# Kernel optimization log

Hardware: AMD Instinct MI355X
Metric: run time of the kernel (lower is better)

Reference implementation:

```python
import jax, jax.numpy as jnp
import numpy as np

D_MODEL = 256
N_HEADS = 8
N_LEVELS = 4
N_POINTS = 4
D_FFN = 1024
HW = 128
LQ = HW * HW
LIN = N_LEVELS * LQ
BATCH = 2
HEAD_DIM = D_MODEL // N_HEADS
SPATIAL = [(HW, HW)] * N_LEVELS  # static (H, W) per level
EPS = 1e-5


def _layer_norm(x, g, b):
    m = jnp.mean(x, axis=-1, keepdims=True)
    v = jnp.mean(jnp.square(x - m), axis=-1, keepdims=True)
    return (x - m) * jax.lax.rsqrt(v + EPS) * g + b


def _gather(v, idx):
    # v: (N, heads, HW, hd); idx: (N, heads, Lq, P) -> (N, heads, Lq, P, hd)
    N, Hh, Lq, P = idx.shape
    out = jnp.take_along_axis(v, idx.reshape(N, Hh, Lq * P)[..., None], axis=2)
    return out.reshape(N, Hh, Lq, P, -1)


def _ms_deform_attn_core(value, loc, attn):
    # value: (N, Lin, heads, hd); loc: (N, Lq, heads, L, P, 2) in [0,1]; attn: (N, Lq, heads, L, P)
    N, _, Hh, hd = value.shape
    Lq = loc.shape[1]
    out = jnp.zeros((N, Hh, Lq, hd), value.dtype)
    start = 0
    for l, (H, W) in enumerate(SPATIAL):
        v = value[:, start:start + H * W].transpose(0, 2, 1, 3)  # (N, heads, H*W, hd)
        start += H * W
        ll = loc[:, :, :, l].transpose(0, 2, 1, 3, 4)  # (N, heads, Lq, P, 2)
        # F.grid_sample(align_corners=False, padding_mode='zeros') on grid 2*loc-1:
        # pixel coord = loc * size - 0.5
        x = ll[..., 0] * W - 0.5
        y = ll[..., 1] * H - 0.5
        x0 = jnp.floor(x)
        y0 = jnp.floor(y)
        wx = x - x0
        wy = y - y0
        x0i = x0.astype(jnp.int32)
        y0i = y0.astype(jnp.int32)
        acc = jnp.zeros((N, Hh, Lq, N_POINTS, hd), value.dtype)
        for dy, wyc in ((0, 1.0 - wy), (1, wy)):
            for dx, wxc in ((0, 1.0 - wx), (1, wx)):
                xi = x0i + dx
                yi = y0i + dy
                valid = (xi >= 0) & (xi < W) & (yi >= 0) & (yi < H)
                idx = jnp.clip(yi, 0, H - 1) * W + jnp.clip(xi, 0, W - 1)
                g = _gather(v, idx)
                w = (wxc * wyc * valid).astype(value.dtype)
                acc = acc + g * w[..., None]
        aw = attn[:, :, :, l].transpose(0, 2, 1, 3)  # (N, heads, Lq, P)
        out = out + jnp.sum(acc * aw[..., None], axis=3)
    return out.transpose(0, 2, 1, 3).reshape(N, Lq, Hh * hd)


def _forward(cur_src, src_all, pos, reference_points, spatial_shape,
             W_off, b_off, W_attn, b_attn, W_val, b_val, W_out, b_out,
             gamma1, beta1, W1, b1, W2, b2, gamma2, beta2):
    N, Lq, d = cur_src.shape
    q = cur_src + pos[:, -1]                      # with_pos_embed(cur_src, pos[-1])
    inp = src_all + pos.reshape(N, -1, d)         # with_pos_embed(src_all, cat(pos, 1))
    value = (inp @ W_val + b_val).reshape(N, -1, N_HEADS, HEAD_DIM)
    off = (q @ W_off + b_off).reshape(N, Lq, N_HEADS, N_LEVELS, N_POINTS, 2)
    attn = (q @ W_attn + b_attn).reshape(N, Lq, N_HEADS, N_LEVELS * N_POINTS)
    attn = jax.nn.softmax(attn, axis=-1).reshape(N, Lq, N_HEADS, N_LEVELS, N_POINTS)
    # offset_normalizer = stack([W, H], -1)
    normalizer = jnp.stack([spatial_shape[..., 1], spatial_shape[..., 0]], -1).astype(cur_src.dtype)
    loc = reference_points[:, :, None, :, None, :] + off / normalizer[None, None, None, :, None, :]
    src2 = _ms_deform_attn_core(value, loc, attn) @ W_out + b_out
    src = _layer_norm(cur_src + src2, gamma1, beta1)   # dropout is identity in eval
    ffn = jax.nn.relu(src @ W1 + b1) @ W2 + b2
    return _layer_norm(src + ffn, gamma2, beta2)


def setup_inputs():
    key = jax.random.key(0)
    ks = jax.random.split(key, 16)
    s = 0.02
    f32 = jnp.float32
    return {
        "cur_src": jax.random.normal(ks[0], (BATCH, LQ, D_MODEL), f32),
        "src_all": jax.random.normal(ks[1], (BATCH, LIN, D_MODEL), f32),
        "pos": jax.random.normal(ks[2], (BATCH, N_LEVELS, LQ, D_MODEL), f32),
        "reference_points": jax.random.uniform(ks[3], (BATCH, LQ, N_LEVELS, 2), f32),
        "spatial_shape": jnp.array(SPATIAL, dtype=jnp.int32),
        "level_start_index": (jnp.arange(N_LEVELS) * LQ).astype(jnp.int32),
        "W_off": jax.random.normal(ks[4], (D_MODEL, N_HEADS * N_LEVELS * N_POINTS * 2), f32) * s,
        "b_off": jax.random.normal(ks[5], (N_HEADS * N_LEVELS * N_POINTS * 2,), f32) * 0.5,
        "W_attn": jax.random.normal(ks[6], (D_MODEL, N_HEADS * N_LEVELS * N_POINTS), f32) * s,
        "b_attn": jnp.zeros((N_HEADS * N_LEVELS * N_POINTS,), f32),
        "W_val": jax.random.normal(ks[7], (D_MODEL, D_MODEL), f32) * s,
        "b_val": jnp.zeros((D_MODEL,), f32),
        "W_out": jax.random.normal(ks[8], (D_MODEL, D_MODEL), f32) * s,
        "b_out": jnp.zeros((D_MODEL,), f32),
        "gamma1": jnp.ones((D_MODEL,), f32),
        "beta1": jnp.zeros((D_MODEL,), f32),
        "W1": jax.random.normal(ks[9], (D_MODEL, D_FFN), f32) * s,
        "b1": jnp.zeros((D_FFN,), f32),
        "W2": jax.random.normal(ks[10], (D_FFN, D_MODEL), f32) * s,
        "b2": jnp.zeros((D_MODEL,), f32),
        "gamma2": jnp.ones((D_MODEL,), f32),
        "beta2": jnp.zeros((D_MODEL,), f32),
    }


def reference(cur_src, src_all, pos, reference_points, spatial_shape, level_start_index,
              W_off, b_off, W_attn, b_attn, W_val, b_val, W_out, b_out,
              gamma1, beta1, W1, b1, W2, b2, gamma2, beta2):
    return _forward(cur_src, src_all, pos, reference_points, spatial_shape,
                    W_off, b_off, W_attn, b_attn, W_val, b_val, W_out, b_out,
                    gamma1, beta1, W1, b1, W2, b2, gamma2, beta2)
```

## Files before the change

kernel.cpp:

```cpp
#include <hip/hip_runtime.h>

#define LQN   16384
#define LINN  65536

typedef __attribute__((ext_vector_type(8))) short bf16x8;
typedef __attribute__((ext_vector_type(4))) float f32x4;
typedef __attribute__((ext_vector_type(4))) unsigned short bf16x4;

__device__ __forceinline__ unsigned short f2bf(float f) {
  unsigned u = __float_as_uint(f);
  u += 0x7FFFu + ((u >> 16) & 1u);
  return (unsigned short)(u >> 16);
}

__global__ __launch_bounds__(256) void wtrans6_kernel(
    const float* __restrict__ Wv, const float* __restrict__ Wo,
    const float* __restrict__ Wa, const float* __restrict__ Wu,
    const float* __restrict__ W1, const float* __restrict__ W2,
    unsigned short* __restrict__ wt) {
  int idx = blockIdx.x * 256 + threadIdx.x;
  const float* W; int K, N, base;
  if (idx < 131072) {
    if (idx < 65536) { W = Wv; K = 256; N = 256; base = 0; }
    else             { W = Wo; K = 256; N = 256; base = 65536; }
  } else if (idx < 229376) {
    if (idx < 163840) { W = Wa; K = 256; N = 128; base = 131072; }
    else              { W = Wu; K = 256; N = 256; base = 163840; }
  } else if (idx < 491520) { W = W1; K = 256; N = 1024; base = 229376; }
  else                     { W = W2; K = 1024; N = 256; base = 491520; }
  int local = idx - base;
  int n = local / K, k = local - n * K;
  wt[idx] = f2bf(W[(size_t)k * N + n]);
}

__global__ __launch_bounds__(256) void addcvt_kernel(
    const float* __restrict__ src_all, const float* __restrict__ pos,
    const float* __restrict__ cur, unsigned short* __restrict__ inp_bf,
    unsigned short* __restrict__ qb) {
  size_t i = (size_t)blockIdx.x * 256 + threadIdx.x;
  if (i < 8388608) {
    float4 a = ((const float4*)src_all)[i];
    float4 b = ((const float4*)pos)[i];
    bf16x4 o;
    o.x = f2bf(a.x + b.x); o.y = f2bf(a.y + b.y);
    o.z = f2bf(a.z + b.z); o.w = f2bf(a.w + b.w);
    ((bf16x4*)inp_bf)[i] = o;
  } else {
    size_t j = i - 8388608;
    size_t row = j >> 6;
    int n = (int)(row >> 14), lq = (int)(row & 16383);
    float4 a = ((const float4*)cur)[j];
    float4 b = ((const float4*)pos)[(((size_t)n * 4 + 3) * LQN + lq) * 64 + (j & 63)];
    bf16x4 o;
    o.x = f2bf(a.x + b.x); o.y = f2bf(a.y + b.y);
    o.z = f2bf(a.z + b.z); o.w = f2bf(a.w + b.w);
    ((bf16x4*)qb)[j] = o;
  }
}

template <int DO_RELU, int OUT_BF16, int SPLIT>
__global__ __launch_bounds__(256) void gemm_lds_kernel(
    const unsigned short* __restrict__ A, const unsigned short* __restrict__ Bt,
    const float* __restrict__ bias, const float* __restrict__ bias2,
    void* __restrict__ Cp, float* __restrict__ Cp2,
    int M, int N, int K, int ny) {
  __shared__ unsigned short As[128 * 64];
  __shared__ unsigned short Bs[128 * 64];
  const int bid = blockIdx.x;
  const int by = bid % ny, bx = bid / ny;
  const int m0 = bx * 128, n0 = by * 128;
  const int tid = threadIdx.x;
  const int wave = tid >> 6, lane = tid & 63;
  const int wm = (wave >> 1) * 64, wn = (wave & 1) * 64;
  const int l15 = lane & 15, quad = lane >> 4;
  const int rl = lane >> 3;
  const int cl = (lane & 7) ^ rl;

  f32x4 acc[4][4];
#pragma unroll
  for (int i = 0; i < 4; i++)
#pragma unroll
    for (int j = 0; j < 4; j++)
#pragma unroll
      for (int r = 0; r < 4; r++) acc[i][j][r] = 0.f;

  const unsigned short* Abase = A + (size_t)m0 * K + cl * 8;
  const unsigned short* Bbase = Bt + (size_t)n0 * K + cl * 8;

  for (int k0 = 0; k0 < K; k0 += 64) {
#pragma unroll
    for (int t = 0; t < 4; t++) {
      const int row = wave * 32 + t * 8 + rl;
      __builtin_amdgcn_global_load_lds(
          (const __attribute__((address_space(1))) void*)(Abase + (size_t)row * K + k0),
          (__attribute__((address_space(3))) void*)(As + (wave * 32 + t * 8) * 64),
          16, 0, 0);
      __builtin_amdgcn_global_load_lds(
          (const __attribute__((address_space(1))) void*)(Bbase + (size_t)row * K + k0),
          (__attribute__((address_space(3))) void*)(Bs + (wave * 32 + t * 8) * 64),
          16, 0, 0);
    }
    __syncthreads();
#pragma unroll
    for (int kk = 0; kk < 2; kk++) {
      bf16x8 af[4], bfr[4];
#pragma unroll
      for (int i = 0; i < 4; i++) {
        const int row = wm + i * 16 + l15;
        af[i] = *(const bf16x8*)&As[row * 64 + (((quad + 4 * kk) ^ (row & 7)) * 8)];
      }
#pragma unroll
      for (int j = 0; j < 4; j++) {
        const int row = wn + j * 16 + l15;
        bfr[j] = *(const bf16x8*)&Bs[row * 64 + (((quad + 4 * kk) ^ (row & 7)) * 8)];
      }
#pragma unroll
      for (int i = 0; i < 4; i++)
#pragma unroll
        for (int j = 0; j < 4; j++)
          acc[i][j] = __builtin_amdgcn_mfma_f32_16x16x32_bf16(af[i], bfr[j], acc[i][j], 0, 0, 0);
    }
    __syncthreads();
  }
#pragma unroll
  for (int i = 0; i < 4; i++) {
#pragma unroll
    for (int j = 0; j < 4; j++) {
      const int col = n0 + wn + j * 16 + l15;
      float bv;
      if (SPLIT) bv = (col < 256) ? bias[col] : bias2[col - 256];
      else       bv = bias[col];
#pragma unroll
      for (int r = 0; r < 4; r++) {
        const int row = m0 + wm + i * 16 + quad * 4 + r;
        float v = acc[i][j][r] + bv;
        if (DO_RELU) v = fmaxf(v, 0.f);
        if (SPLIT) {
          if (col < 256) ((float*)Cp)[(size_t)row * 256 + col] = v;
          else           Cp2[(size_t)row * 128 + (col - 256)] = v;
        } else if (OUT_BF16) {
          ((unsigned short*)Cp)[(size_t)row * N + col] = f2bf(v);
        } else {
          ((float*)Cp)[(size_t)row * N + col] = v;
        }
      }
    }
  }
}

__global__ __launch_bounds__(256) void sample_kernel(
    const unsigned short* __restrict__ value, const float* __restrict__ offs,
    const float* __restrict__ attnl, const float* __restrict__ refp,
    unsigned int* __restrict__ attn_out) {
  const int tid = threadIdx.x;
  const int sub = tid >> 4;
  const int c = tid & 15;
  const int g = blockIdx.x * 16 + sub;
  const int n = g >> 17;
  const int nl = g >> 3;
  const int h = g & 7;

  const float* lg = attnl + (size_t)nl * 128 + h * 16;
  float e[16];
  float mx = -1e30f;
#pragma unroll
  for (int i = 0; i < 16; i++) { e[i] = lg[i]; mx = fmaxf(mx, e[i]); }
  float s = 0.f;
#pragma unroll
  for (int i = 0; i < 16; i++) { e[i] = __expf(e[i] - mx); s += e[i]; }
  const float inv = 1.f / s;

  const int pt = c;
  const int pl = pt >> 2;
  const float ox = offs[((size_t)g * 16 + pt) * 2 + 0];
  const float oy = offs[((size_t)g * 16 + pt) * 2 + 1];
  const float rx = refp[((size_t)nl * 4 + pl) * 2 + 0];
  const float ry = refp[((size_t)nl * 4 + pl) * 2 + 1];
  const float x = fmaf(rx, 128.f, ox - 0.5f);
  const float y = fmaf(ry, 128.f, oy - 0.5f);
  const float xf = floorf(x), yf = floorf(y);
  const float fx = x - xf, fy = y - yf;
  const int x0 = (int)xf, y0 = (int)yf;
  const float aw = e[pt] * inv;
  const int xc0 = min(max(x0, 0), 127), xc1 = min(max(x0 + 1, 0), 127);
  const int yc0 = min(max(y0, 0), 127), yc1 = min(max(y0 + 1, 0), 127);
  float wx0 = (x0 >= 0 && x0 <= 127) ? (1.f - fx) : 0.f;
  float wx1 = (x0 >= -1 && x0 <= 126) ? fx : 0.f;
  float wy0 = ((y0 >= 0 && y0 <= 127) ? (1.f - fy) : 0.f) * aw;
  float wy1 = ((y0 >= -1 && y0 <= 126) ? fy : 0.f) * aw;
  const int packed = xc0 | (xc1 << 7) | (yc0 << 14) | (yc1 << 21);

  const unsigned int* base0 =
      (const unsigned int*)value + (((size_t)n * LINN) * 8 + h) * 16 + c;

  float a0 = 0.f, a1 = 0.f;
#pragma unroll
  for (int p = 0; p < 16; p++) {
    const int pk = __shfl(packed, p, 16);
    const float w_x0 = __shfl(wx0, p, 16);
    const float w_x1 = __shfl(wx1, p, 16);
    const float w_y0 = __shfl(wy0, p, 16);
    const float w_y1 = __shfl(wy1, p, 16);
    const unsigned int* bl = base0 + (size_t)(p >> 2) * (LQN * 128);
    const int X0 = pk & 127, X1 = (pk >> 7) & 127;
    const int Y0 = (pk >> 14) & 127, Y1 = (pk >> 21) & 127;
    const unsigned v00 = bl[(Y0 * 128 + X0) * 128];
    const unsigned v01 = bl[(Y0 * 128 + X1) * 128];
    const unsigned v10 = bl[(Y1 * 128 + X0) * 128];
    const unsigned v11 = bl[(Y1 * 128 + X1) * 128];
    const float w00 = w_x0 * w_y0, w01 = w_x1 * w_y0;
    const float w10 = w_x0 * w_y1, w11 = w_x1 * w_y1;
    a0 = fmaf(w00, __uint_as_float(v00 << 16), a0);
    a1 = fmaf(w00, __uint_as_float(v00 & 0xFFFF0000u), a1);
    a0 = fmaf(w01, __uint_as_float(v01 << 16), a0);
    a1 = fmaf(w01, __uint_as_float(v01 & 0xFFFF0000u), a1);
    a0 = fmaf(w10, __uint_as_float(v10 << 16), a0);
    a1 = fmaf(w10, __uint_as_float(v10 & 0xFFFF0000u), a1);
    a0 = fmaf(w11, __uint_as_float(v11 << 16), a0);
    a1 = fmaf(w11, __uint_as_float(v11 & 0xFFFF0000u), a1);
  }
  attn_out[(size_t)g * 16 + c] = (unsigned)f2bf(a0) | ((unsigned)f2bf(a1) << 16);
}

template <int EMIT_BF16>
__global__ __launch_bounds__(256) void ln_kernel(const float* __restrict__ x1,
                                                 const float* __restrict__ x2,
                                                 const float* __restrict__ gamma,
                                                 const float* __restrict__ beta,
                                                 float* __restrict__ out,
                                                 unsigned short* __restrict__ outb) {
  const int row = blockIdx.x * 4 + (threadIdx.x >> 6);
  const int lane = threadIdx.x & 63;
  float4 a = ((const float4*)(x1 + (size_t)row * 256))[lane];
  float4 b = ((const float4*)(x2 + (size_t)row * 256))[lane];
  float v0 = a.x + b.x, v1 = a.y + b.y, v2 = a.z + b.z, v3 = a.w + b.w;
  float s1 = v0 + v1 + v2 + v3;
  float s2 = v0 * v0 + v1 * v1 + v2 * v2 + v3 * v3;
#pragma unroll
  for (int o = 1; o < 64; o <<= 1) { s1 += __shfl_xor(s1, o); s2 += __shfl_xor(s2, o); }
  const float mean = s1 * (1.f / 256.f);
  const float var = s2 * (1.f / 256.f) - mean * mean;
  const float rstd = rsqrtf(var + 1e-5f);
  float4 gm = ((const float4*)gamma)[lane];
  float4 bt = ((const float4*)beta)[lane];
  float4 o4;
  o4.x = (v0 - mean) * rstd * gm.x + bt.x;
  o4.y = (v1 - mean) * rstd * gm.y + bt.y;
  o4.z = (v2 - mean) * rstd * gm.z + bt.z;
  o4.w = (v3 - mean) * rstd * gm.w + bt.w;
  ((float4*)(out + (size_t)row * 256))[lane] = o4;
  if (EMIT_BF16) {
    bf16x4 ob;
    ob.x = f2bf(o4.x); ob.y = f2bf(o4.y); ob.z = f2bf(o4.z); ob.w = f2bf(o4.w);
    ((bf16x4*)(outb + (size_t)row * 256))[lane] = ob;
  }
}

extern "C" void kernel_launch(void* const* d_in, const int* in_sizes, int n_in,
                              void* d_out, int out_size, void* d_ws, size_t ws_size,
                              hipStream_t stream) {
  (void)in_sizes; (void)n_in; (void)out_size; (void)ws_size;
  const float* cur_src = (const float*)d_in[0];
  const float* src_all = (const float*)d_in[1];
  const float* pos     = (const float*)d_in[2];
  const float* refp    = (const float*)d_in[3];
  const float* W_off   = (const float*)d_in[6];
  const float* b_off   = (const float*)d_in[7];
  const float* W_attn  = (const float*)d_in[8];
  const float* b_attn  = (const float*)d_in[9];
  const float* W_val   = (const float*)d_in[10];
  const float* b_val   = (const float*)d_in[11];
  const float* W_out   = (const float*)d_in[12];
  const float* b_out   = (const float*)d_in[13];
  const float* gamma1  = (const float*)d_in[14];
  const float* beta1   = (const float*)d_in[15];
  const float* W1      = (const float*)d_in[16];
  const float* b1      = (const float*)d_in[17];
  const float* W2      = (const float*)d_in[18];
  const float* b2      = (const float*)d_in[19];
  const float* gamma2  = (const float*)d_in[20];
  const float* beta2   = (const float*)d_in[21];
  float* out = (float*)d_out;

  char* ws = (char*)d_ws;
  unsigned short* value = (unsigned short*)(ws + 0);
  unsigned short* qbuf  = (unsigned short*)(ws + 67108864);
  float* offbuf         = (float*)(ws + 83886080);
  float* attnl          = (float*)(ws + 117440512);
  unsigned short* attno = (unsigned short*)(ws + 134217728);
  float* src2           = (float*)(ws + 150994944);
  float* srcb           = (float*)(ws + 184549376);
  unsigned short* wt    = (unsigned short*)(ws + 218103808);
  unsigned short* wt_val  = wt;
  unsigned short* wt_qa   = wt + 65536;
  unsigned short* wt_out  = wt + 163840;
  unsigned short* wt_1    = wt + 229376;
  unsigned short* wt_2    = wt + 491520;
  unsigned short* srcb_bf = (unsigned short*)attnl;
  unsigned short* inp_bf  = (unsigned short*)src2;

  wtrans6_kernel<<<2944, 256, 0, stream>>>(W_val, W_off, W_attn, W_out, W1, W2, wt);

  addcvt_kernel<<<40960, 256, 0, stream>>>(src_all, pos, cur_src, inp_bf, qbuf);

  gemm_lds_kernel<0, 1, 0><<<2048, 256, 0, stream>>>(
      inp_bf, wt_val, b_val, nullptr, value, nullptr, 131072, 256, 256, 2);
  gemm_lds_kernel<0, 0, 1><<<768, 256, 0, stream>>>(
      qbuf, wt_qa, b_off, b_attn, offbuf, attnl, 32768, 384, 256, 3);
  sample_kernel<<<16384, 256, 0, stream>>>(value, offbuf, attnl, refp,
                                           (unsigned int*)attno);
  gemm_lds_kernel<0, 0, 0><<<512, 256, 0, stream>>>(
      attno, wt_out, b_out, nullptr, src2, nullptr, 32768, 256, 256, 2);
  ln_kernel<1><<<8192, 256, 0, stream>>>(cur_src, src2, gamma1, beta1, srcb, srcb_bf);
  gemm_lds_kernel<1, 1, 0><<<2048, 256, 0, stream>>>(
      srcb_bf, wt_1, b1, nullptr, value, nullptr, 32768, 1024, 256, 8);
  gemm_lds_kernel<0, 0, 0><<<512, 256, 0, stream>>>(
      value, wt_2, b2, nullptr, offbuf, nullptr, 32768, 256, 1024, 2);
  ln_kernel<0><<<8192, 256, 0, stream>>>(srcb, offbuf, gamma2, beta2, out, nullptr);
}
```

Before: 643.4 us.

## Restructure deformable sampling to 8 lanes per head with LDS-staged weights and wider loads

The sampling kernel now assigns 8 lanes per (query, head), each handling 4 channels with 8-byte loads. Per-point bilinear weights and packed corner indices are staged in LDS instead of being broadcast through shuffles, and softmax is computed by a cooperative shuffle reduction. The goal is fewer load instructions and less shuffle/ALU overhead on the gather-bound stage. The add-and-convert kernel also reuses the already-loaded pos value for the query buffer, which removes a separate grid region and a second pos read, at the cost of some added LDS use.

```diff
diff --git a/kernel.cpp b/kernel.cpp
--- a/kernel.cpp
+++ b/kernel.cpp
@@ -38,23 +38,20 @@
     const float* __restrict__ cur, unsigned short* __restrict__ inp_bf,
     unsigned short* __restrict__ qb) {
   size_t i = (size_t)blockIdx.x * 256 + threadIdx.x;
-  if (i < 8388608) {
-    float4 a = ((const float4*)src_all)[i];
-    float4 b = ((const float4*)pos)[i];
-    bf16x4 o;
-    o.x = f2bf(a.x + b.x); o.y = f2bf(a.y + b.y);
-    o.z = f2bf(a.z + b.z); o.w = f2bf(a.w + b.w);
-    ((bf16x4*)inp_bf)[i] = o;
-  } else {
-    size_t j = i - 8388608;
-    size_t row = j >> 6;
-    int n = (int)(row >> 14), lq = (int)(row & 16383);
-    float4 a = ((const float4*)cur)[j];
-    float4 b = ((const float4*)pos)[(((size_t)n * 4 + 3) * LQN + lq) * 64 + (j & 63)];
-    bf16x4 o;
-    o.x = f2bf(a.x + b.x); o.y = f2bf(a.y + b.y);
-    o.z = f2bf(a.z + b.z); o.w = f2bf(a.w + b.w);
-    ((bf16x4*)qb)[j] = o;
+  float4 a = ((const float4*)src_all)[i];
+  float4 b = ((const float4*)pos)[i];
+  bf16x4 o;
+  o.x = f2bf(a.x + b.x); o.y = f2bf(a.y + b.y);
+  o.z = f2bf(a.z + b.z); o.w = f2bf(a.w + b.w);
+  ((bf16x4*)inp_bf)[i] = o;
+  size_t m = i & 4194303;
+  if (m >= 3145728) {
+    size_t jq = (i >> 22) * 1048576 + (m - 3145728);
+    float4 cc = ((const float4*)cur)[jq];
+    bf16x4 o2;
+    o2.x = f2bf(cc.x + b.x); o2.y = f2bf(cc.y + b.y);
+    o2.z = f2bf(cc.z + b.z); o2.w = f2bf(cc.w + b.w);
+    ((bf16x4*)qb)[jq] = o2;
   }
 }
 
@@ -152,74 +149,87 @@
     const unsigned short* __restrict__ value, const float* __restrict__ offs,
     const float* __restrict__ attnl, const float* __restrict__ refp,
     unsigned int* __restrict__ attn_out) {
+  __shared__ float wlds[32 * 16 * 8];
   const int tid = threadIdx.x;
-  const int sub = tid >> 4;
-  const int c = tid & 15;
-  const int g = blockIdx.x * 16 + sub;
+  const int sub = tid >> 3;
+  const int cl  = tid & 7;
+  const int g = blockIdx.x * 32 + sub;
   const int n = g >> 17;
   const int nl = g >> 3;
   const int h = g & 7;
 
   const float* lg = attnl + (size_t)nl * 128 + h * 16;
-  float e[16];
-  float mx = -1e30f;
-#pragma unroll
-  for (int i = 0; i < 16; i++) { e[i] = lg[i]; mx = fmaxf(mx, e[i]); }
-  float s = 0.f;
-#pragma unroll
-  for (int i = 0; i < 16; i++) { e[i] = __expf(e[i] - mx); s += e[i]; }
+  const float2 l2 = *(const float2*)(lg + 2 * cl);
+  float mx = fmaxf(l2.x, l2.y);
+#pragma unroll
+  for (int o = 1; o < 8; o <<= 1) mx = fmaxf(mx, __shfl_xor(mx, o, 8));
+  const float e0 = __expf(l2.x - mx), e1 = __expf(l2.y - mx);
+  float s = e0 + e1;
+#pragma unroll
+  for (int o = 1; o < 8; o <<= 1) s += __shfl_xor(s, o, 8);
   const float inv = 1.f / s;
 
-  const int pt = c;
-  const int pl = pt >> 2;
-  const float ox = offs[((size_t)g * 16 + pt) * 2 + 0];
-  const float oy = offs[((size_t)g * 16 + pt) * 2 + 1];
-  const float rx = refp[((size_t)nl * 4 + pl) * 2 + 0];
-  const float ry = refp[((size_t)nl * 4 + pl) * 2 + 1];
-  const float x = fmaf(rx, 128.f, ox - 0.5f);
-  const float y = fmaf(ry, 128.f, oy - 0.5f);
-  const float xf = floorf(x), yf = floorf(y);
-  const float fx = x - xf, fy = y - yf;
-  const int x0 = (int)xf, y0 = (int)yf;
-  const float aw = e[pt] * inv;
-  const int xc0 = min(max(x0, 0), 127), xc1 = min(max(x0 + 1, 0), 127);
-  const int yc0 = min(max(y0, 0), 127), yc1 = min(max(y0 + 1, 0), 127);
-  float wx0 = (x0 >= 0 && x0 <= 127) ? (1.f - fx) : 0.f;
-  float wx1 = (x0 >= -1 && x0 <= 126) ? fx : 0.f;
-  float wy0 = ((y0 >= 0 && y0 <= 127) ? (1.f - fy) : 0.f) * aw;
-  float wy1 = ((y0 >= -1 && y0 <= 126) ? fy : 0.f) * aw;
-  const int packed = xc0 | (xc1 << 7) | (yc0 << 14) | (yc1 << 21);
-
-  const unsigned int* base0 =
-      (const unsigned int*)value + (((size_t)n * LINN) * 8 + h) * 16 + c;
-
-  float a0 = 0.f, a1 = 0.f;
+  const float4 o4 = *(const float4*)(offs + (size_t)g * 32 + 4 * cl);
+  const float2 r2 = *(const float2*)(refp + ((size_t)nl * 4 + (cl >> 1)) * 2);
+#pragma unroll
+  for (int q = 0; q < 2; q++) {
+    const float ox = (q == 0) ? o4.x : o4.z;
+    const float oy = (q == 0) ? o4.y : o4.w;
+    const float aw = ((q == 0) ? e0 : e1) * inv;
+    const float x = fmaf(r2.x, 128.f, ox - 0.5f);
+    const float y = fmaf(r2.y, 128.f, oy - 0.5f);
+    const float xf = floorf(x), yf = floorf(y);
+    const float fx = x - xf, fy = y - yf;
+    const int x0 = (int)xf, y0 = (int)yf;
+    const int xc0 = min(max(x0, 0), 127), xc1 = min(max(x0 + 1, 0), 127);
+    const int yc0 = min(max(y0, 0), 127), yc1 = min(max(y0 + 1, 0), 127);
+    const float wx0 = (x0 >= 0 && x0 <= 127) ? (1.f - fx) : 0.f;
+    const float wx1 = (x0 >= -1 && x0 <= 126) ? fx : 0.f;
+    const float wy0 = ((y0 >= 0 && y0 <= 127) ? (1.f - fy) : 0.f) * aw;
+    const float wy1 = ((y0 >= -1 && y0 <= 126) ? fy : 0.f) * aw;
+    const int p00 = yc0 * 128 + xc0;
+    const int p11 = yc1 * 128 + xc1;
+    const int dxp = xc1 - xc0;
+    const unsigned pk = (unsigned)p00 | ((unsigned)p11 << 14) | ((unsigned)dxp << 28);
+    const int pt = 2 * cl + q;
+    float4 w4;
+    w4.x = wx0 * wy0; w4.y = wx1 * wy0; w4.z = wx0 * wy1; w4.w = wx1 * wy1;
+    *(float4*)&wlds[(sub * 16 + pt) * 8] = w4;
+    wlds[(sub * 16 + pt) * 8 + 4] = __uint_as_float(pk);
+  }
+
+  const char* vb = (const char*)value;
+  const unsigned baseidx = ((unsigned)n << 23) + (unsigned)(h * 16 + 2 * cl);
+  float a0 = 0.f, a1 = 0.f, a2 = 0.f, a3 = 0.f;
 #pragma unroll
   for (int p = 0; p < 16; p++) {
-    const int pk = __shfl(packed, p, 16);
-    const float w_x0 = __shfl(wx0, p, 16);
-    const float w_x1 = __shfl(wx1, p, 16);
-    const float w_y0 = __shfl(wy0, p, 16);
-    const float w_y1 = __shfl(wy1, p, 16);
-    const unsigned int* bl = base0 + (size_t)(p >> 2) * (LQN * 128);
-    const int X0 = pk & 127, X1 = (pk >> 7) & 127;
-    const int Y0 = (pk >> 14) & 127, Y1 = (pk >> 21) & 127;
-    const unsigned v00 = bl[(Y0 * 128 + X0) * 128];
-    const unsigned v01 = bl[(Y0 * 128 + X1) * 128];
-    const unsigned v10 = bl[(Y1 * 128 + X0) * 128];
-    const unsigned v11 = bl[(Y1 * 128 + X1) * 128];
-    const float w00 = w_x0 * w_y0, w01 = w_x1 * w_y0;
-    const float w10 = w_x0 * w_y1, w11 = w_x1 * w_y1;
-    a0 = fmaf(w00, __uint_as_float(v00 << 16), a0);
-    a1 = fmaf(w00, __uint_as_float(v00 & 0xFFFF0000u), a1);
-    a0 = fmaf(w01, __uint_as_float(v01 << 16), a0);
-    a1 = fmaf(w01, __uint_as_float(v01 & 0xFFFF0000u), a1);
-    a0 = fmaf(w10, __uint_as_float(v10 << 16), a0);
-    a1 = fmaf(w10, __uint_as_float(v10 & 0xFFFF0000u), a1);
-    a0 = fmaf(w11, __uint_as_float(v11 << 16), a0);
-    a1 = fmaf(w11, __uint_as_float(v11 & 0xFFFF0000u), a1);
-  }
-  attn_out[(size_t)g * 16 + c] = (unsigned)f2bf(a0) | ((unsigned)f2bf(a1) << 16);
+    const float4 w4 = *(const float4*)&wlds[(sub * 16 + p) * 8];
+    const unsigned pk = __float_as_uint(wlds[(sub * 16 + p) * 8 + 4]);
+    const unsigned lb = (unsigned)(p >> 2) * 2097152u;
+    const unsigned p00 = pk & 16383u;
+    const unsigned p11 = (pk >> 14) & 16383u;
+    const unsigned d128 = (pk >> 28) << 7;
+    const unsigned iA = baseidx + (lb + p00 * 128u);
+    const unsigned iB = baseidx + (lb + p11 * 128u);
+    const uint2 v00 = *(const uint2*)(vb + ((iA) << 2));
+    const uint2 v01 = *(const uint2*)(vb + ((iA + d128) << 2));
+    const uint2 v11 = *(const uint2*)(vb + ((iB) << 2));
+    const uint2 v10 = *(const uint2*)(vb + ((iB - d128) << 2));
+#define ACC4(vv, w)                                             \
+    a0 = fmaf(w, __uint_as_float((vv).x << 16), a0);            \
+    a1 = fmaf(w, __uint_as_float((vv).x & 0xFFFF0000u), a1);    \
+    a2 = fmaf(w, __uint_as_float((vv).y << 16), a2);            \
+    a3 = fmaf(w, __uint_as_float((vv).y & 0xFFFF0000u), a3);
+    ACC4(v00, w4.x)
+    ACC4(v01, w4.y)
+    ACC4(v10, w4.z)
+    ACC4(v11, w4.w)
+#undef ACC4
+  }
+  uint2 o;
+  o.x = (unsigned)f2bf(a0) | ((unsigned)f2bf(a1) << 16);
+  o.y = (unsigned)f2bf(a2) | ((unsigned)f2bf(a3) << 16);
+  ((uint2*)attn_out)[(size_t)g * 8 + cl] = o;
 }
 
 template <int EMIT_BF16>
@@ -301,14 +311,14 @@
 
   wtrans6_kernel<<<2944, 256, 0, stream>>>(W_val, W_off, W_attn, W_out, W1, W2, wt);
 
-  addcvt_kernel<<<40960, 256, 0, stream>>>(src_all, pos, cur_src, inp_bf, qbuf);
+  addcvt_kernel<<<32768, 256, 0, stream>>>(src_all, pos, cur_src, inp_bf, qbuf);
 
   gemm_lds_kernel<0, 1, 0><<<2048, 256, 0, stream>>>(
       inp_bf, wt_val, b_val, nullptr, value, nullptr, 131072, 256, 256, 2);
   gemm_lds_kernel<0, 0, 1><<<768, 256, 0, stream>>>(
       qbuf, wt_qa, b_off, b_attn, offbuf, attnl, 32768, 384, 256, 3);
-  sample_kernel<<<16384, 256, 0, stream>>>(value, offbuf, attnl, refp,
-                                           (unsigned int*)attno);
+  sample_kernel<<<8192, 256, 0, stream>>>(value, offbuf, attnl, refp,
+                                          (unsigned int*)attno);
   gemm_lds_kernel<0, 0, 0><<<512, 256, 0, stream>>>(
       attno, wt_out, b_out, nullptr, src2, nullptr, 32768, 256, 256, 2);
   ln_kernel<1><<<8192, 256, 0, stream>>>(cur_src, src2, gamma1, beta1, srcb, srcb_bf);
```

After: 652.9 us. No clear change (+1.5%).
